# Performance work log

Hardware: AMD Instinct MI355X
Metric: run time of the kernel (lower is better)

The kernel has to match this reference:

```python
import jax, jax.numpy as jnp
import numpy as np

EPS = 1e-6
COST_CLASS = 1.0
COST_MASK = 1.0
COST_DICE = 1.0


def setup_inputs() -> dict:
    key = jax.random.key(0)
    k1, k2, k3, k4 = jax.random.split(key, 4)
    bs, Q, T, H, W, C = 4, 100, 25, 256, 256, 81
    pred_logits = jax.random.normal(k1, (bs, Q, C), dtype=jnp.float32)
    pred_masks = jax.random.normal(k2, (bs, Q, H, W), dtype=jnp.float32)
    tgt_labels = jax.random.randint(k3, (bs, T), 0, C, dtype=jnp.int64)
    tgt_masks = jax.random.uniform(k4, (bs, T, H, W), dtype=jnp.float32)
    return {
        'pred_logits': pred_logits,
        'pred_masks': pred_masks,
        'tgt_labels': tgt_labels,
        'tgt_masks': tgt_masks,
    }


def reference(pred_logits, pred_masks, tgt_labels, tgt_masks):
    # pred_logits: [bs, Q, C]; pred_masks: [bs, Q, H, W] (logits)
    # tgt_labels:  [bs, T] int; tgt_masks: [bs, T, H, W] in [0,1]
    bs, Q = pred_masks.shape[:2]
    T = tgt_masks.shape[1]
    P = pred_masks.shape[-2] * pred_masks.shape[-1]

    x = pred_masks.reshape(bs, Q, P)   # mask logits
    y = tgt_masks.reshape(bs, T, P)    # target masks

    # classification cost: -softmax(prob)[:, tgt_ids]
    prob = jax.nn.softmax(pred_logits, axis=-1)                 # [bs, Q, C]
    cost_class = -jnp.take_along_axis(prob, tgt_labels[:, None, :], axis=2)  # [bs, Q, T]

    # pairwise mean BCE-with-logits:
    #   BCE(x, y) = softplus(x) - x*y, averaged over pixels
    #   -> mean_p softplus(x_qp)  (per query)  -  (x @ y^T) / P
    softplus_mean = jnp.mean(jax.nn.softplus(x), axis=-1)       # [bs, Q]
    xy = jnp.einsum('bqp,btp->bqt', x, y)                       # [bs, Q, T]
    bce_matrix = softplus_mean[..., None] - xy / P

    # pairwise dice cost
    sig = jax.nn.sigmoid(x)                                     # [bs, Q, P]
    numerator = 2.0 * jnp.einsum('bqp,btp->bqt', sig, y)        # [bs, Q, T]
    denominator = sig.sum(-1)[..., None] + y.sum(-1)[:, None, :] + EPS
    dice_matrix = 1.0 - numerator / denominator

    C = COST_CLASS * cost_class + COST_MASK * bce_matrix + COST_DICE * dice_matrix
    return C  # [bs, Q, T]; Hungarian assignment (scipy) runs on this CPU-side
```

## Files before the change

### kernel.cpp

```cpp
#include <hip/hip_runtime.h>

#define BS 4
#define NQ 100
#define NT 25
#define NC 81
#define PIX 65536
#define KCHUNK 512
#define NKB (PIX / KCHUNK)
#define NQT 7
#define STRY 520

#define WS_SP 0
#define WS_SG 400
#define WS_YT 800
#define WS_P0 1024
#define PSZ   (BS * NQT * NKB * 400)
#define WS_P1 (WS_P0 + PSZ)

typedef __attribute__((ext_vector_type(8))) short bf16x8;
typedef __attribute__((ext_vector_type(4))) float f32x4;

__device__ __forceinline__ float4 ld4(const float* p) {
    return *reinterpret_cast<const float4*>(p);
}
__device__ __forceinline__ f32x4 mfma16(bf16x8 a, bf16x8 b, f32x4 c) {
    return __builtin_amdgcn_mfma_f32_16x16x32_bf16(a, b, c, 0, 0, 0);
}
__device__ __forceinline__ unsigned pack2t(float lo, float hi) {
#if __has_builtin(__builtin_amdgcn_perm)
    return __builtin_amdgcn_perm(__float_as_uint(hi), __float_as_uint(lo), 0x07060302u);
#else
    return (__float_as_uint(hi) & 0xFFFF0000u) | (__float_as_uint(lo) >> 16);
#endif
}
__device__ __forceinline__ unsigned pack2r(float lo, float hi) {
#if __has_builtin(__builtin_amdgcn_perm)
    return __builtin_amdgcn_perm(__float_as_uint(hi) + 0x8000u,
                                 __float_as_uint(lo) + 0x8000u, 0x07060302u);
#else
    return (((__float_as_uint(hi) + 0x8000u) & 0xFFFF0000u) |
            ((__float_as_uint(lo) + 0x8000u) >> 16));
#endif
}

union frag_u { unsigned u[4]; bf16x8 v; };

__global__ __launch_bounds__(256) void partial_kernel(
    const float* __restrict__ pm,
    const float* __restrict__ tm,
    float* __restrict__ ws)
{
    __shared__ unsigned short ys[32 * STRY];

    const int tid = threadIdx.x;
    const int bid = blockIdx.x;
    const int chunk = bid & (NKB - 1);
    const int rest = bid >> 7;
    const int qg = rest & 1;
    const int b = rest >> 1;
    const int kbase = chunk * KCHUNK;

    {
        const float* yg = tm + (size_t)b * NT * PIX + kbase;
        for (int j = tid; j < 32 * (KCHUNK / 4); j += 256) {
            const int row = j >> 7, c = j & 127;
            uint2 w = make_uint2(0u, 0u);
            if (row < NT) {
                const float4 v = ld4(yg + (size_t)row * PIX + c * 4);
                w.x = pack2r(v.x, v.y);
                w.y = pack2r(v.z, v.w);
            }
            *reinterpret_cast<uint2*>(&ys[row * STRY + c * 4]) = w;
        }
    }
    __syncthreads();

    const int l = tid & 63;
    const int wv = tid >> 6;
    const int qt = qg * 4 + wv;
    const bool ones_wave = (qt == 7);
    const int lrow = l & 15;
    const int lk = (l >> 4) * 8;

    const int q = qt * 16 + lrow;
    const bool qv = (q < NQ);

    const float* xp = pm + (size_t)(b * NQ + (qv ? q : 0)) * PIX + kbase + lk;

    f32x4 cxy[2] = {};
    f32x4 csy[2] = {};
    float sx = 0.f, sg = 0.f, l2 = 0.f;

    frag_u fones;
    fones.u[0] = fones.u[1] = fones.u[2] = fones.u[3] = 0x3F803F80u;

    float4 Xa[2], Xb[2];
    if (!ones_wave) {
        Xa[0] = ld4(xp);      Xb[0] = ld4(xp + 4);
        Xa[1] = ld4(xp + 32); Xb[1] = ld4(xp + 36);
    }

    bf16x8 by0 = *reinterpret_cast<const bf16x8*>(&ys[lrow * STRY + lk]);
    bf16x8 by1 = *reinterpret_cast<const bf16x8*>(&ys[(16 + lrow) * STRY + lk]);

    #pragma unroll
    for (int kb = 0; kb < KCHUNK / 32; ++kb) {
        bf16x8 nb0, nb1;
        if (kb < KCHUNK / 32 - 1) {
            const int ko = (kb + 1) * 32;
            nb0 = *reinterpret_cast<const bf16x8*>(&ys[lrow * STRY + ko + lk]);
            nb1 = *reinterpret_cast<const bf16x8*>(&ys[(16 + lrow) * STRY + ko + lk]);
        }

        frag_u fx, fs;
        if (!ones_wave) {
            const float4 xa = Xa[kb & 1], xb = Xb[kb & 1];
            if (kb < KCHUNK / 32 - 2) {
                const int ko = (kb + 2) * 32;
                Xa[kb & 1] = ld4(xp + ko);
                Xb[kb & 1] = ld4(xp + ko + 4);
            }
            const float xe[8] = {xa.x, xa.y, xa.z, xa.w, xb.x, xb.y, xb.z, xb.w};
            float rg[8];
            float pr = 1.0f;
            #pragma unroll
            for (int e = 0; e < 8; ++e) {
                const float x = xe[e];
                const float ex = __expf(-x);
                const float r = __builtin_amdgcn_rcpf(1.0f + ex);
                rg[e] = r;
                pr *= r;
                sx += x;
                sg += r;
            }
            l2 += __log2f(pr);
            #pragma unroll
            for (int e = 0; e < 4; ++e) {
                fx.u[e] = pack2t(xe[2 * e], xe[2 * e + 1]);
                fs.u[e] = pack2t(rg[2 * e], rg[2 * e + 1]);
            }
        } else {
            fx = fones; fs = fones;
        }

        cxy[0] = mfma16(fx.v, by0, cxy[0]);
        cxy[1] = mfma16(fx.v, by1, cxy[1]);
        csy[0] = mfma16(fs.v, by0, csy[0]);
        csy[1] = mfma16(fs.v, by1, csy[1]);

        if (kb < KCHUNK / 32 - 1) { by0 = nb0; by1 = nb1; }
    }

    if (!ones_wave) {
        const size_t slot = ((size_t)(b * NQT + qt) * NKB + chunk) * 400;
        float* px = ws + WS_P0 + slot;
        float* ps = ws + WS_P1 + slot;
        #pragma unroll
        for (int n = 0; n < 2; ++n) {
            const int t = n * 16 + lrow;
            if (t < NT) {
                #pragma unroll
                for (int r = 0; r < 4; ++r) {
                    const int qr = (l >> 4) * 4 + r;
                    px[qr * NT + t] = cxy[n][r];
                    ps[qr * NT + t] = csy[n][r];
                }
            }
        }
        sx += __shfl_xor(sx, 16); sx += __shfl_xor(sx, 32);
        l2 += __shfl_xor(l2, 16); l2 += __shfl_xor(l2, 32);
        sg += __shfl_xor(sg, 16); sg += __shfl_xor(sg, 32);
        if (l < 16 && qv) {
            atomicAdd(&ws[WS_SP + b * NQ + q], sx - 0.69314718056f * l2);
            atomicAdd(&ws[WS_SG + b * NQ + q], sg);
        }
    } else {
        if (l < 16) atomicAdd(&ws[WS_YT + b * NT + l], cxy[0][0]);
        if (l < NT - 16) atomicAdd(&ws[WS_YT + b * NT + 16 + l], cxy[1][0]);
    }
}

__global__ __launch_bounds__(256) void finalize_kernel(
    const float* __restrict__ logits,
    const int* __restrict__ labels,
    const float* __restrict__ ws,
    float* __restrict__ out)
{
    __shared__ float s1[256];
    __shared__ float s2[256];

    const int row = blockIdx.x;
    const int b = row / NQ, q = row % NQ;
    const int qt = q / 16, qr = q % 16;
    const int tid = threadIdx.x;
    const int t = tid & 31, cg = tid >> 5;

    float sxy = 0.f, ssy = 0.f;
    if (t < NT) {
        const size_t base = ((size_t)(b * NQT + qt) * NKB) * 400 + (size_t)qr * NT + t;
        const float* px = ws + WS_P0 + base;
        const float* ps = ws + WS_P1 + base;
        #pragma unroll 4
        for (int k = 0; k < NKB / 8; ++k) {
            const size_t o = (size_t)(cg + 8 * k) * 400;
            sxy += px[o];
            ssy += ps[o];
        }
    }
    s1[tid] = sxy;
    s2[tid] = ssy;
    __syncthreads();

    if (tid < 64) {
        const float* lg = logits + (size_t)row * NC;
        float v0 = (tid < NC) ? lg[tid] : -1e30f;
        float v1 = (tid + 64 < NC) ? lg[tid + 64] : -1e30f;
        float mx = fmaxf(v0, v1);
        #pragma unroll
        for (int off = 32; off; off >>= 1) mx = fmaxf(mx, __shfl_xor(mx, off, 64));
        float e = ((tid < NC) ? __expf(v0 - mx) : 0.f) +
                  ((tid + 64 < NC) ? __expf(v1 - mx) : 0.f);
        #pragma unroll
        for (int off = 32; off; off >>= 1) e += __shfl_xor(e, off, 64);

        if (tid < NT) {
            float xy = 0.f, sy = 0.f;
            #pragma unroll
            for (int g = 0; g < 8; ++g) { xy += s1[g * 32 + tid]; sy += s2[g * 32 + tid]; }

            const int lab = labels[b * NT + tid];
            const float prob = __expf(lg[lab] - mx) / e;
            const float inv_p = 1.0f / (float)PIX;
            const float bce = ws[WS_SP + row] * inv_p - xy * inv_p;
            const float dice = 1.0f - 2.0f * sy /
                               (ws[WS_SG + row] + ws[WS_YT + b * NT + tid] + 1e-6f);
            out[(size_t)row * NT + tid] = -prob + bce + dice;
        }
    }
}

extern "C" void kernel_launch(void* const* d_in, const int* in_sizes, int n_in,
                              void* d_out, int out_size, void* d_ws, size_t ws_size,
                              hipStream_t stream) {
    const float* pred_logits = (const float*)d_in[0];
    const float* pred_masks  = (const float*)d_in[1];
    const int*   tgt_labels  = (const int*)d_in[2];
    const float* tgt_masks   = (const float*)d_in[3];
    float* out = (float*)d_out;
    float* ws  = (float*)d_ws;

    hipMemsetAsync(d_ws, 0, 1024 * sizeof(float), stream);

    partial_kernel<<<BS * 2 * NKB, 256, 0, stream>>>(pred_masks, tgt_masks, ws);
    finalize_kernel<<<BS * NQ, 256, 0, stream>>>(pred_logits, tgt_labels, ws, out);
}
```

Measured before the change: 47.23 us.

## Compute per-query x and sigmoid sums via MFMA against ones; deepen X prefetch

Replaces the per-element scalar accumulation of x and sigmoid(x) with two extra MFMAs that multiply the packed bf16 fragments by a ones matrix, then writes those row sums through atomics from lane-column 0. The global prefetch of pred_masks is deepened from two to three stages using a modulo-3 slot. This trades VALU adds for matrix-core work and more registers. The sums now come from bf16-truncated values, so there is a precision risk. The atomic pattern also changes.

```diff
diff --git a/kernel.cpp b/kernel.cpp
--- a/kernel.cpp
+++ b/kernel.cpp
@@ -89,15 +89,18 @@
 
     f32x4 cxy[2] = {};
     f32x4 csy[2] = {};
-    float sx = 0.f, sg = 0.f, l2 = 0.f;
+    f32x4 cxs = {};
+    f32x4 css = {};
+    float l2 = 0.f;
 
     frag_u fones;
     fones.u[0] = fones.u[1] = fones.u[2] = fones.u[3] = 0x3F803F80u;
 
-    float4 Xa[2], Xb[2];
+    float4 Xa[3], Xb[3];
     if (!ones_wave) {
         Xa[0] = ld4(xp);      Xb[0] = ld4(xp + 4);
         Xa[1] = ld4(xp + 32); Xb[1] = ld4(xp + 36);
+        Xa[2] = ld4(xp + 64); Xb[2] = ld4(xp + 68);
     }
 
     bf16x8 by0 = *reinterpret_cast<const bf16x8*>(&ys[lrow * STRY + lk]);
@@ -114,11 +117,12 @@
 
         frag_u fx, fs;
         if (!ones_wave) {
-            const float4 xa = Xa[kb & 1], xb = Xb[kb & 1];
-            if (kb < KCHUNK / 32 - 2) {
-                const int ko = (kb + 2) * 32;
-                Xa[kb & 1] = ld4(xp + ko);
-                Xb[kb & 1] = ld4(xp + ko + 4);
+            const int slot = kb % 3;
+            const float4 xa = Xa[slot], xb = Xb[slot];
+            if (kb < KCHUNK / 32 - 3) {
+                const int ko = (kb + 3) * 32;
+                Xa[slot] = ld4(xp + ko);
+                Xb[slot] = ld4(xp + ko + 4);
             }
             const float xe[8] = {xa.x, xa.y, xa.z, xa.w, xb.x, xb.y, xb.z, xb.w};
             float rg[8];
@@ -130,8 +134,6 @@
                 const float r = __builtin_amdgcn_rcpf(1.0f + ex);
                 rg[e] = r;
                 pr *= r;
-                sx += x;
-                sg += r;
             }
             l2 += __log2f(pr);
             #pragma unroll
@@ -147,6 +149,10 @@
         cxy[1] = mfma16(fx.v, by1, cxy[1]);
         csy[0] = mfma16(fs.v, by0, csy[0]);
         csy[1] = mfma16(fs.v, by1, csy[1]);
+        if (!ones_wave) {
+            cxs = mfma16(fx.v, fones.v, cxs);
+            css = mfma16(fs.v, fones.v, css);
+        }
 
         if (kb < KCHUNK / 32 - 1) { by0 = nb0; by1 = nb1; }
     }
@@ -167,12 +173,19 @@
                 }
             }
         }
-        sx += __shfl_xor(sx, 16); sx += __shfl_xor(sx, 32);
         l2 += __shfl_xor(l2, 16); l2 += __shfl_xor(l2, 32);
-        sg += __shfl_xor(sg, 16); sg += __shfl_xor(sg, 32);
         if (l < 16 && qv) {
-            atomicAdd(&ws[WS_SP + b * NQ + q], sx - 0.69314718056f * l2);
-            atomicAdd(&ws[WS_SG + b * NQ + q], sg);
+            atomicAdd(&ws[WS_SP + b * NQ + q], -0.69314718056f * l2);
+        }
+        if ((l & 15) == 0) {
+            #pragma unroll
+            for (int r = 0; r < 4; ++r) {
+                const int qq = qt * 16 + (l >> 4) * 4 + r;
+                if (qq < NQ) {
+                    atomicAdd(&ws[WS_SP + b * NQ + qq], cxs[r]);
+                    atomicAdd(&ws[WS_SG + b * NQ + qq], css[r]);
+                }
+            }
         }
     } else {
         if (l < 16) atomicAdd(&ws[WS_YT + b * NT + l], cxy[0][0]);
```

Measured after the change: 76.16 us. 1.61x slower.
